# Optimization experiments

Hardware: AMD Instinct MI355X
Metric: run time of the kernel (lower is better)

Reference implementation:

```python
import jax, jax.numpy as jnp
import numpy as np

B, T, C, N = 64, 2048, 1, 128  # batch, max seq len, num_conjugates, num_tags


def setup_inputs() -> dict:
    key = jax.random.key(0)
    k1, k2, k3, k4, k5 = jax.random.split(key, 5)
    emissions = jax.random.normal(k1, (B, T, C, N), dtype=jnp.float32)
    # ragged lengths in [T//2, T], guaranteed >= 1
    token_sizes = jax.random.randint(k2, (B,), T // 2, T + 1, dtype=jnp.int32)
    # learned CRF parameters (torch init is zeros; use small random for a nontrivial baseline)
    transitions = 0.1 * jax.random.normal(k3, (1, C, N, N), dtype=jnp.float32)
    head_transitions = 0.1 * jax.random.normal(k4, (1, C, N), dtype=jnp.float32)
    last_transitions = 0.1 * jax.random.normal(k5, (1, C, N), dtype=jnp.float32)
    return {
        "emissions": emissions,
        "token_sizes": token_sizes,
        "transitions": transitions,
        "head_transitions": head_transitions,
        "last_transitions": last_transitions,
    }


def _log_partition(emissions, transitions, head_transitions, last_transitions, token_sizes):
    # emissions: [B, T, C, N]; transitions: [1, C, N, N]; head/last: [1, C, N]
    trans = transitions[0]  # [C, N, N]
    # alpha_0 = head_transitions (*) emissions[0] in the Log semiring
    alpha0 = head_transitions[0][None, :, :] + emissions[:, 0]  # [B, C, N]

    def step(alpha, inp):
        em_t, t = inp  # em_t: [B, C, N], t: scalar time index
        # Log-semiring matmul: logsumexp over previous tag
        new = jax.nn.logsumexp(alpha[:, :, :, None] + trans[None, :, :, :], axis=2) + em_t
        valid = (t < token_sizes)[:, None, None]  # mask padded steps (identity in semiring)
        return jnp.where(valid, new, alpha), None

    step = jax.checkpoint(step)
    xs = (jnp.swapaxes(emissions[:, 1:], 0, 1), jnp.arange(1, emissions.shape[1]))
    alpha, _ = jax.lax.scan(step, alpha0, xs)
    # terminate with last_transitions, reduce over final tag
    return jax.nn.logsumexp(alpha + last_transitions[0][None, :, :], axis=-1)  # [B, C]


def reference(emissions, token_sizes, transitions, head_transitions, last_transitions):
    return _log_partition(emissions, transitions, head_transitions, last_transitions, token_sizes)
```

## Files before the change

kernel.cpp:

```cpp
#include <hip/hip_runtime.h>
#include <stdint.h>

#define T_LEN 2048
#define B_TOT 64
#define N_TAG 128
#define MID 1024

typedef __attribute__((ext_vector_type(4))) float f32x4;
typedef __attribute__((ext_vector_type(8))) short bf16x8;
typedef __attribute__((ext_vector_type(4))) uint32_t u32x4;
typedef __attribute__((ext_vector_type(2))) uint32_t u32x2;

template <int S>
struct IC {
  static constexpr int value = S;
};

__device__ __align__(16) float g_alpha[B_TOT][N_TAG];
__device__ __align__(16) float g_v[B_TOT][N_TAG];
__device__ float g_Lf[B_TOT];
__device__ float g_Lb[B_TOT];
__device__ int g_done = 0;

__device__ __forceinline__ uint32_t pack2_bf16(float a, float b) {
  uint32_t ua = __float_as_uint(a) + 0x8000u;
  uint32_t ub = __float_as_uint(b) + 0x8000u;
  return __builtin_amdgcn_perm(ua, ub, 0x03020706u);
}

__global__ __launch_bounds__(512, 2) void crf_scan_kernel(
    const float* __restrict__ em, const int* __restrict__ lens,
    const float* __restrict__ trans, const float* __restrict__ head,
    const float* __restrict__ last, float* __restrict__ out) {
  const int lane = threadIdx.x & 63;
  const int w = threadIdx.x >> 6;
  const int f = w >> 1;
  const int h = w & 1;
  const int c = lane & 15;
  const int q = lane >> 4;
  const bool is_fwd = (blockIdx.x < 4);
  const int bg = ((int)blockIdx.x & 3) * 16 + c;
  const int jbase = f * 32 + q * 8 + h * 4;

  __shared__ uint32_t x_lds[2][4][64][4];
  __shared__ int k_lds[16];
  __shared__ int ticket_lds;

  const float* eptr = em + (size_t)bg * T_LEN * N_TAG + jbase;
  f32x4 eslot[8];
  auto issue_eem = [&](auto sc, int row) {
    constexpr int S = decltype(sc)::value;
    eslot[S] = *(const f32x4*)(eptr + (size_t)row * N_TAG);
  };

  const f32x4 vzero = {0.f, 0.f, 0.f, 0.f};

  if (is_fwd) {
    bf16x8 efrag[4];
    {
      const int j = f * 32 + (c >> 2) * 8 + h * 4 + (c & 3);
#pragma unroll
      for (int ktv = 0; ktv < 4; ++ktv) {
        const int ktp = (w + ktv) & 3;
        u32x4 wd;
#pragma unroll
        for (int p = 0; p < 4; ++p) {
          const int i0 = ktp * 32 + q * 8 + 2 * p;
          wd[p] = pack2_bf16(__expf(trans[(i0 + 0) * N_TAG + j]),
                             __expf(trans[(i0 + 1) * N_TAG + j]));
        }
        efrag[ktv] = __builtin_bit_cast(bf16x8, wd);
      }
    }
    float L = 0.f;
    {
      float v0[4];
#pragma unroll
      for (int r = 0; r < 4; ++r) v0[r] = __expf(head[jbase + r] + eptr[r]);
      u32x2 wd;
      wd[0] = pack2_bf16(v0[0], v0[1]);
      wd[1] = pack2_bf16(v0[2], v0[3]);
      *(u32x2*)&x_lds[0][f][lane][h * 2] = wd;
    }
    if (w == 0 && lane < 16) k_lds[lane] = 0;
    __syncthreads();

    issue_eem(IC<1>{}, 1);
    issue_eem(IC<2>{}, 2);
    issue_eem(IC<3>{}, 3);
    issue_eem(IC<4>{}, 4);
    issue_eem(IC<5>{}, 5);
    issue_eem(IC<6>{}, 6);
    issue_eem(IC<7>{}, 7);

    auto step = [&](auto slotc, int t) {
      constexpr int SLOT = decltype(slotc)::value;
      constexpr int RP = (SLOT + 1) & 1;
      constexpr int WP = SLOT & 1;
      issue_eem(IC<(SLOT + 7) & 7>{}, t + 7);
      int e = 0;
      if ((SLOT & 3) == 1) e = k_lds[c];
      u32x4 bfr[4];
#pragma unroll
      for (int ktv = 0; ktv < 4; ++ktv)
        bfr[ktv] = *(const u32x4*)&x_lds[RP][(w + ktv) & 3][lane][0];
      const f32x4 ev = eslot[SLOT];
      float ff[4];
#pragma unroll
      for (int r = 0; r < 4; ++r) ff[r] = __expf(ev[r]);
      if ((SLOT & 3) == 1) {
        const float sc = __uint_as_float((uint32_t)(127 - e) << 23);
#pragma unroll
        for (int r = 0; r < 4; ++r) ff[r] *= sc;
        L += (float)e * 0.6931471805599453f;
      }
      f32x4 a0 = __builtin_amdgcn_mfma_f32_16x16x32_bf16(
          efrag[0], __builtin_bit_cast(bf16x8, bfr[0]), vzero, 0, 0, 0);
      f32x4 a1 = __builtin_amdgcn_mfma_f32_16x16x32_bf16(
          efrag[2], __builtin_bit_cast(bf16x8, bfr[2]), vzero, 0, 0, 0);
      a0 = __builtin_amdgcn_mfma_f32_16x16x32_bf16(
          efrag[1], __builtin_bit_cast(bf16x8, bfr[1]), a0, 0, 0, 0);
      a1 = __builtin_amdgcn_mfma_f32_16x16x32_bf16(
          efrag[3], __builtin_bit_cast(bf16x8, bfr[3]), a1, 0, 0, 0);
      const f32x4 acc = a0 + a1;
      if ((SLOT & 3) == 0) {
        if (w == 0 && lane < 16)
          k_lds[c] = (int)(__float_as_uint(acc[0]) >> 23) - 126;
      }
      if (t == MID - 1) {
#pragma unroll
        for (int r = 0; r < 4; ++r) g_alpha[bg][jbase + r] = acc[r] * ff[r];
        if (w == 0 && q == 0) g_Lf[bg] = L;
      }
      u32x2 wd;
      wd[0] = pack2_bf16(acc[0] * ff[0], acc[1] * ff[1]);
      wd[1] = pack2_bf16(acc[2] * ff[2], acc[3] * ff[3]);
      *(u32x2*)&x_lds[WP][f][lane][h * 2] = wd;
      __syncthreads();
    };

    int t = 1;
#pragma unroll 1
    for (int it = 0; it < 127; ++it) {
      step(IC<1>{}, t);
      step(IC<2>{}, t + 1);
      step(IC<3>{}, t + 2);
      step(IC<4>{}, t + 3);
      step(IC<5>{}, t + 4);
      step(IC<6>{}, t + 5);
      step(IC<7>{}, t + 6);
      step(IC<0>{}, t + 7);
      t += 8;
    }
    step(IC<1>{}, t);
    step(IC<2>{}, t + 1);
    step(IC<3>{}, t + 2);
    step(IC<4>{}, t + 3);
    step(IC<5>{}, t + 4);
    step(IC<6>{}, t + 5);
    step(IC<7>{}, t + 6);
  } else {
    bf16x8 efrag[4];
    {
      const int irow = f * 32 + (c >> 2) * 8 + h * 4 + (c & 3);
#pragma unroll
      for (int ktv = 0; ktv < 4; ++ktv) {
        const int ktp = (w + ktv) & 3;
        u32x4 wd;
#pragma unroll
        for (int p = 0; p < 4; ++p) {
          const int j0 = ktp * 32 + q * 8 + 2 * p;
          wd[p] = pack2_bf16(__expf(trans[irow * N_TAG + j0 + 0]),
                             __expf(trans[irow * N_TAG + j0 + 1]));
        }
        efrag[ktv] = __builtin_bit_cast(bf16x8, wd);
      }
    }
    const int mylen = lens[bg];
    float L = 0.f;
    float vprev[4];
    {
#pragma unroll
      for (int r = 0; r < 4; ++r) vprev[r] = __expf(last[jbase + r]);
      float e0[4];
#pragma unroll
      for (int r = 0; r < 4; ++r)
        e0[r] = __expf(eptr[(size_t)(T_LEN - 1) * N_TAG + r]);
      u32x2 wd;
      wd[0] = pack2_bf16(vprev[0] * e0[0], vprev[1] * e0[1]);
      wd[1] = pack2_bf16(vprev[2] * e0[2], vprev[3] * e0[3]);
      *(u32x2*)&x_lds[0][f][lane][h * 2] = wd;
    }
    if (w == 0 && lane < 16) k_lds[lane] = 0;
    __syncthreads();

    issue_eem(IC<1>{}, T_LEN - 2);
    issue_eem(IC<2>{}, T_LEN - 3);
    issue_eem(IC<3>{}, T_LEN - 4);
    issue_eem(IC<4>{}, T_LEN - 5);
    issue_eem(IC<5>{}, T_LEN - 6);
    issue_eem(IC<6>{}, T_LEN - 7);
    issue_eem(IC<7>{}, T_LEN - 8);

    auto step = [&](auto slotc, int t) {
      constexpr int SLOT = decltype(slotc)::value;
      constexpr int RP = (SLOT + 1) & 1;
      constexpr int WP = SLOT & 1;
      issue_eem(IC<(SLOT + 7) & 7>{}, t - 8);
      int e = 0;
      if ((SLOT & 3) == 1) e = k_lds[c];
      u32x4 bfr[4];
#pragma unroll
      for (int ktv = 0; ktv < 4; ++ktv)
        bfr[ktv] = *(const u32x4*)&x_lds[RP][(w + ktv) & 3][lane][0];
      const f32x4 ev = eslot[SLOT];
      float ee[4];
#pragma unroll
      for (int r = 0; r < 4; ++r) ee[r] = __expf(ev[r]);
      f32x4 a0 = __builtin_amdgcn_mfma_f32_16x16x32_bf16(
          efrag[0], __builtin_bit_cast(bf16x8, bfr[0]), vzero, 0, 0, 0);
      f32x4 a1 = __builtin_amdgcn_mfma_f32_16x16x32_bf16(
          efrag[2], __builtin_bit_cast(bf16x8, bfr[2]), vzero, 0, 0, 0);
      a0 = __builtin_amdgcn_mfma_f32_16x16x32_bf16(
          efrag[1], __builtin_bit_cast(bf16x8, bfr[1]), a0, 0, 0, 0);
      a1 = __builtin_amdgcn_mfma_f32_16x16x32_bf16(
          efrag[3], __builtin_bit_cast(bf16x8, bfr[3]), a1, 0, 0, 0);
      const f32x4 acc = a0 + a1;
      const bool valid = (t < mylen);
      float vnew[4];
#pragma unroll
      for (int r = 0; r < 4; ++r) vnew[r] = valid ? acc[r] : vprev[r];
      if ((SLOT & 3) == 1) {
        const float sc = __uint_as_float((uint32_t)(127 - e) << 23);
#pragma unroll
        for (int r = 0; r < 4; ++r) vnew[r] *= sc;
        L += (float)e * 0.6931471805599453f;
      }
      if ((SLOT & 3) == 0) {
        if (w == 0 && lane < 16)
          k_lds[c] = (int)(__float_as_uint(vnew[0]) >> 23) - 126;
      }
      if (t == MID) {
#pragma unroll
        for (int r = 0; r < 4; ++r) g_v[bg][jbase + r] = vnew[r];
        if (w == 0 && q == 0) g_Lb[bg] = L;
      }
      u32x2 wd;
      wd[0] = pack2_bf16(vnew[0] * ee[0], vnew[1] * ee[1]);
      wd[1] = pack2_bf16(vnew[2] * ee[2], vnew[3] * ee[3]);
      *(u32x2*)&x_lds[WP][f][lane][h * 2] = wd;
#pragma unroll
      for (int r = 0; r < 4; ++r) vprev[r] = vnew[r];
      __syncthreads();
    };

    int t = T_LEN - 1;
#pragma unroll 1
    for (int it = 0; it < 128; ++it) {
      step(IC<1>{}, t);
      step(IC<2>{}, t - 1);
      step(IC<3>{}, t - 2);
      step(IC<4>{}, t - 3);
      step(IC<5>{}, t - 4);
      step(IC<6>{}, t - 5);
      step(IC<7>{}, t - 6);
      step(IC<0>{}, t - 7);
      t -= 8;
    }
  }

  __threadfence();
  if (threadIdx.x == 0) ticket_lds = atomicAdd(&g_done, 1);
  __syncthreads();
  if (ticket_lds == 7) {
    __threadfence();
    const int b = threadIdx.x >> 3;
    const int p = threadIdx.x & 7;
    float s = 0.f;
#pragma unroll
    for (int k = 0; k < 4; ++k) {
      const f32x4 a = *(const f32x4*)&g_alpha[b][p * 16 + k * 4];
      const f32x4 v = *(const f32x4*)&g_v[b][p * 16 + k * 4];
      s += a[0] * v[0] + a[1] * v[1] + a[2] * v[2] + a[3] * v[3];
    }
    s += __shfl_xor(s, 1);
    s += __shfl_xor(s, 2);
    s += __shfl_xor(s, 4);
    if (p == 0) out[b] = __logf(s) + g_Lf[b] + g_Lb[b];
    __syncthreads();
    if (threadIdx.x == 0) atomicExch(&g_done, 0);
  }
}

extern "C" void kernel_launch(void* const* d_in, const int* in_sizes, int n_in,
                              void* d_out, int out_size, void* d_ws,
                              size_t ws_size, hipStream_t stream) {
  const float* em = (const float*)d_in[0];
  const int* lens = (const int*)d_in[1];
  const float* trans = (const float*)d_in[2];
  const float* head = (const float*)d_in[3];
  const float* last = (const float*)d_in[4];
  float* out = (float*)d_out;
  (void)d_ws;
  (void)ws_size;

  crf_scan_kernel<<<8, 512, 0, stream>>>(em, lens, trans, head, last, out);
}
```

Before: 341.6 us.

## Precompute exp(emissions) as bf16 in producer blocks overlapped with the scan

Adds 256 producer blocks to the launch. They exponentiate emissions, pack them to bf16 into a workspace laid out time-major, and publish per-chunk completion counters. The 8 scan blocks spin-wait on those counters and then load the half-size precomputed values, which removes the per-step exp and halves the streamed bytes on the serial critical path. The risks are spin-wait stalls if the producers fall behind, possible deadlock if a scan block waits on producers that are not yet resident, and extra bf16 rounding of the emission factors.

Measured after the change: 395.1 us. 1.16x slower.

```diff
diff --git a/kernel.cpp b/kernel.cpp
--- a/kernel.cpp
+++ b/kernel.cpp
@@ -21,17 +21,52 @@
 __device__ float g_Lf[B_TOT];
 __device__ float g_Lb[B_TOT];
 __device__ int g_done = 0;
+__device__ int g_chunk_rows[16];
 
 __device__ __forceinline__ uint32_t pack2_bf16(float a, float b) {
   uint32_t ua = __float_as_uint(a) + 0x8000u;
   uint32_t ub = __float_as_uint(b) + 0x8000u;
   return __builtin_amdgcn_perm(ua, ub, 0x03020706u);
 }
-
-__global__ __launch_bounds__(512, 2) void crf_scan_kernel(
+__device__ __forceinline__ float bf_lo(uint32_t w) {
+  return __uint_as_float(w << 16);
+}
+__device__ __forceinline__ float bf_hi(uint32_t w) {
+  return __uint_as_float(w & 0xffff0000u);
+}
+
+__global__ __launch_bounds__(512, 2) void crf_fused_kernel(
     const float* __restrict__ em, const int* __restrict__ lens,
     const float* __restrict__ trans, const float* __restrict__ head,
-    const float* __restrict__ last, float* __restrict__ out) {
+    const float* __restrict__ last, uint32_t* __restrict__ eem,
+    float* __restrict__ out) {
+  if (blockIdx.x >= 8) {
+    const int p = (int)blockIdx.x - 8;
+    const int start = (p & 1) ? 2040 - (p >> 1) * 8 : (p >> 1) * 8;
+    const int tid = threadIdx.x;
+#pragma unroll 1
+    for (int u = 0; u < 16; ++u) {
+      const int row = start + (u >> 1);
+      const int unit = (u & 1) * 512 + tid;
+      const int b = unit >> 4;
+      const int kk = unit & 15;
+      const float4* src =
+          (const float4*)(em + ((size_t)b * T_LEN + row) * N_TAG + kk * 8);
+      const float4 p0 = src[0];
+      const float4 p1 = src[1];
+      u32x4 o;
+      o[0] = pack2_bf16(__expf(p0.x), __expf(p0.y));
+      o[1] = pack2_bf16(__expf(p0.z), __expf(p0.w));
+      o[2] = pack2_bf16(__expf(p1.x), __expf(p1.y));
+      o[3] = pack2_bf16(__expf(p1.z), __expf(p1.w));
+      *(u32x4*)(eem + (size_t)row * 4096 + b * 64 + kk * 4) = o;
+    }
+    __syncthreads();
+    __threadfence();
+    if (tid == 0) atomicAdd(&g_chunk_rows[start >> 7], 8);
+    return;
+  }
+
   const int lane = threadIdx.x & 63;
   const int w = threadIdx.x >> 6;
   const int f = w >> 1;
@@ -46,11 +81,21 @@
   __shared__ int k_lds[16];
   __shared__ int ticket_lds;
 
+  auto wait_chunk = [&](int ch) {
+    if (threadIdx.x == 0) {
+      while (__hip_atomic_load(&g_chunk_rows[ch], __ATOMIC_ACQUIRE,
+                               __HIP_MEMORY_SCOPE_AGENT) < 128) {
+      }
+    }
+    __syncthreads();
+  };
+
   const float* eptr = em + (size_t)bg * T_LEN * N_TAG + jbase;
-  f32x4 eslot[8];
+  const uint32_t* eqp = eem + (size_t)bg * 64 + f * 16 + q * 4 + h * 2;
+  u32x2 eslot[8];
   auto issue_eem = [&](auto sc, int row) {
     constexpr int S = decltype(sc)::value;
-    eslot[S] = *(const f32x4*)(eptr + (size_t)row * N_TAG);
+    eslot[S] = *(const u32x2*)(eqp + (size_t)row * 4096);
   };
 
   const f32x4 vzero = {0.f, 0.f, 0.f, 0.f};
@@ -85,6 +130,7 @@
     if (w == 0 && lane < 16) k_lds[lane] = 0;
     __syncthreads();
 
+    wait_chunk(0);
     issue_eem(IC<1>{}, 1);
     issue_eem(IC<2>{}, 2);
     issue_eem(IC<3>{}, 3);
@@ -104,10 +150,12 @@
 #pragma unroll
       for (int ktv = 0; ktv < 4; ++ktv)
         bfr[ktv] = *(const u32x4*)&x_lds[RP][(w + ktv) & 3][lane][0];
-      const f32x4 ev = eslot[SLOT];
+      const u32x2 ev = eslot[SLOT];
       float ff[4];
-#pragma unroll
-      for (int r = 0; r < 4; ++r) ff[r] = __expf(ev[r]);
+      ff[0] = bf_lo(ev[0]);
+      ff[1] = bf_hi(ev[0]);
+      ff[2] = bf_lo(ev[1]);
+      ff[3] = bf_hi(ev[1]);
       if ((SLOT & 3) == 1) {
         const float sc = __uint_as_float((uint32_t)(127 - e) << 23);
 #pragma unroll
@@ -140,8 +188,14 @@
     };
 
     int t = 1;
+    int cur_ch = 0;
 #pragma unroll 1
     for (int it = 0; it < 127; ++it) {
+      const int ch = (15 + 8 * it) >> 7;
+      if (ch != cur_ch) {
+        wait_chunk(ch);
+        cur_ch = ch;
+      }
       step(IC<1>{}, t);
       step(IC<2>{}, t + 1);
       step(IC<3>{}, t + 2);
@@ -152,6 +206,7 @@
       step(IC<0>{}, t + 7);
       t += 8;
     }
+    wait_chunk(8);
     step(IC<1>{}, t);
     step(IC<2>{}, t + 1);
     step(IC<3>{}, t + 2);
@@ -194,6 +249,7 @@
     if (w == 0 && lane < 16) k_lds[lane] = 0;
     __syncthreads();
 
+    wait_chunk(15);
     issue_eem(IC<1>{}, T_LEN - 2);
     issue_eem(IC<2>{}, T_LEN - 3);
     issue_eem(IC<3>{}, T_LEN - 4);
@@ -213,10 +269,12 @@
 #pragma unroll
       for (int ktv = 0; ktv < 4; ++ktv)
         bfr[ktv] = *(const u32x4*)&x_lds[RP][(w + ktv) & 3][lane][0];
-      const f32x4 ev = eslot[SLOT];
+      const u32x2 ev = eslot[SLOT];
       float ee[4];
-#pragma unroll
-      for (int r = 0; r < 4; ++r) ee[r] = __expf(ev[r]);
+      ee[0] = bf_lo(ev[0]);
+      ee[1] = bf_hi(ev[0]);
+      ee[2] = bf_lo(ev[1]);
+      ee[3] = bf_hi(ev[1]);
       f32x4 a0 = __builtin_amdgcn_mfma_f32_16x16x32_bf16(
           efrag[0], __builtin_bit_cast(bf16x8, bfr[0]), vzero, 0, 0, 0);
       f32x4 a1 = __builtin_amdgcn_mfma_f32_16x16x32_bf16(
@@ -255,8 +313,14 @@
     };
 
     int t = T_LEN - 1;
+    int cur_ch = 15;
 #pragma unroll 1
     for (int it = 0; it < 128; ++it) {
+      const int ch = (2032 - 8 * it) >> 7;
+      if (ch != cur_ch) {
+        wait_chunk(ch);
+        cur_ch = ch;
+      }
       step(IC<1>{}, t);
       step(IC<2>{}, t - 1);
       step(IC<3>{}, t - 2);
@@ -288,7 +352,8 @@
     s += __shfl_xor(s, 4);
     if (p == 0) out[b] = __logf(s) + g_Lf[b] + g_Lb[b];
     __syncthreads();
-    if (threadIdx.x == 0) atomicExch(&g_done, 0);
+    if (threadIdx.x == 0) g_done = 0;
+    if (threadIdx.x < 16) g_chunk_rows[threadIdx.x] = 0;
   }
 }
 
@@ -301,8 +366,8 @@
   const float* head = (const float*)d_in[3];
   const float* last = (const float*)d_in[4];
   float* out = (float*)d_out;
-  (void)d_ws;
-  (void)ws_size;
-
-  crf_scan_kernel<<<8, 512, 0, stream>>>(em, lens, trans, head, last, out);
-}
+  uint32_t* ws = (uint32_t*)d_ws;
+
+  crf_fused_kernel<<<264, 512, 0, stream>>>(em, lens, trans, head, last, ws,
+                                            out);
+}
```

## Precompute exp(emissions) as bf16 in a prepass and halve scan block waves

Applied to the files above, without the earlier changes.

Adds a parallel prepass kernel that computes exp of every emission, packs it to bf16 and writes it time-major into the workspace. The sequential scan kernel then loads half the bytes per step and skips the per-step exp. The scan block also drops from 8 to 4 waves, each doing 8 MFMAs per step over 32 tags, so fewer waves take part in each per-step barrier. The costs are an extra launch, a full pass over the emissions, and emission values rounded to bf16 before the multiply.

New measurement: 412.6 us. 1.21x slower.

```diff
diff --git a/kernel.cpp b/kernel.cpp
--- a/kernel.cpp
+++ b/kernel.cpp
@@ -27,41 +27,65 @@
   uint32_t ub = __float_as_uint(b) + 0x8000u;
   return __builtin_amdgcn_perm(ua, ub, 0x03020706u);
 }
-
-__global__ __launch_bounds__(512, 2) void crf_scan_kernel(
+__device__ __forceinline__ float bf_lo(uint32_t w) {
+  return __uint_as_float(w << 16);
+}
+__device__ __forceinline__ float bf_hi(uint32_t w) {
+  return __uint_as_float(w & 0xffff0000u);
+}
+
+__global__ __launch_bounds__(256) void eem_prepass(const float* __restrict__ em,
+                                                   uint32_t* __restrict__ ws) {
+  const int tid = blockIdx.x * blockDim.x + threadIdx.x;
+  const int b = tid >> 15;
+  const int rem = tid & 32767;
+  const int t = rem >> 4;
+  const int kk = rem & 15;
+  const float4* src =
+      (const float4*)(em + ((size_t)b * T_LEN + t) * N_TAG + kk * 8);
+  const float4 p0 = src[0];
+  const float4 p1 = src[1];
+  u32x4 o;
+  o[0] = pack2_bf16(__expf(p0.x), __expf(p0.y));
+  o[1] = pack2_bf16(__expf(p0.z), __expf(p0.w));
+  o[2] = pack2_bf16(__expf(p1.x), __expf(p1.y));
+  o[3] = pack2_bf16(__expf(p1.z), __expf(p1.w));
+  *(u32x4*)(ws + ((size_t)t * B_TOT + b) * (N_TAG / 2) + kk * 4) = o;
+}
+
+__global__ __launch_bounds__(256, 1) void crf_scan_kernel(
     const float* __restrict__ em, const int* __restrict__ lens,
     const float* __restrict__ trans, const float* __restrict__ head,
-    const float* __restrict__ last, float* __restrict__ out) {
+    const float* __restrict__ last, const uint32_t* __restrict__ eem,
+    float* __restrict__ out) {
   const int lane = threadIdx.x & 63;
   const int w = threadIdx.x >> 6;
-  const int f = w >> 1;
-  const int h = w & 1;
   const int c = lane & 15;
   const int q = lane >> 4;
   const bool is_fwd = (blockIdx.x < 4);
   const int bg = ((int)blockIdx.x & 3) * 16 + c;
-  const int jbase = f * 32 + q * 8 + h * 4;
+  const int jb = w * 32 + q * 8;
 
   __shared__ uint32_t x_lds[2][4][64][4];
   __shared__ int k_lds[16];
   __shared__ int ticket_lds;
 
-  const float* eptr = em + (size_t)bg * T_LEN * N_TAG + jbase;
-  f32x4 eslot[8];
+  const uint32_t* eqp = eem + (size_t)bg * 64 + w * 16 + q * 4;
+  u32x4 eslot[8];
   auto issue_eem = [&](auto sc, int row) {
     constexpr int S = decltype(sc)::value;
-    eslot[S] = *(const f32x4*)(eptr + (size_t)row * N_TAG);
+    eslot[S] = *(const u32x4*)(eqp + (size_t)row * 4096);
   };
 
   const f32x4 vzero = {0.f, 0.f, 0.f, 0.f};
 
   if (is_fwd) {
-    bf16x8 efrag[4];
-    {
-      const int j = f * 32 + (c >> 2) * 8 + h * 4 + (c & 3);
-#pragma unroll
-      for (int ktv = 0; ktv < 4; ++ktv) {
-        const int ktp = (w + ktv) & 3;
+    bf16x8 efrag[2][4];
+#pragma unroll
+    for (int mt = 0; mt < 2; ++mt) {
+      const int j = w * 32 + (c >> 2) * 8 + mt * 4 + (c & 3);
+#pragma unroll
+      for (int ktp = 0; ktp < 4; ++ktp) {
         u32x4 wd;
 #pragma unroll
         for (int p = 0; p < 4; ++p) {
@@ -69,18 +93,19 @@
           wd[p] = pack2_bf16(__expf(trans[(i0 + 0) * N_TAG + j]),
                              __expf(trans[(i0 + 1) * N_TAG + j]));
         }
-        efrag[ktv] = __builtin_bit_cast(bf16x8, wd);
+        efrag[mt][ktp] = __builtin_bit_cast(bf16x8, wd);
       }
     }
     float L = 0.f;
     {
-      float v0[4];
-#pragma unroll
-      for (int r = 0; r < 4; ++r) v0[r] = __expf(head[jbase + r] + eptr[r]);
-      u32x2 wd;
-      wd[0] = pack2_bf16(v0[0], v0[1]);
-      wd[1] = pack2_bf16(v0[2], v0[3]);
-      *(u32x2*)&x_lds[0][f][lane][h * 2] = wd;
+      const float* emb = em + (size_t)bg * T_LEN * N_TAG;
+      float v0[8];
+#pragma unroll
+      for (int r = 0; r < 8; ++r) v0[r] = __expf(head[jb + r] + emb[jb + r]);
+      u32x4 wd;
+#pragma unroll
+      for (int d = 0; d < 4; ++d) wd[d] = pack2_bf16(v0[2 * d], v0[2 * d + 1]);
+      *(u32x4*)&x_lds[0][w][lane][0] = wd;
     }
     if (w == 0 && lane < 16) k_lds[lane] = 0;
     __syncthreads();
@@ -97,45 +122,74 @@
       constexpr int SLOT = decltype(slotc)::value;
       constexpr int RP = (SLOT + 1) & 1;
       constexpr int WP = SLOT & 1;
-      issue_eem(IC<(SLOT + 7) & 7>{}, t + 7);
+      {
+        int row = t + 7;
+        if (row > T_LEN - 1) row = T_LEN - 1;
+        issue_eem(IC<(SLOT + 7) & 7>{}, row);
+      }
       int e = 0;
       if ((SLOT & 3) == 1) e = k_lds[c];
       u32x4 bfr[4];
 #pragma unroll
       for (int ktv = 0; ktv < 4; ++ktv)
         bfr[ktv] = *(const u32x4*)&x_lds[RP][(w + ktv) & 3][lane][0];
-      const f32x4 ev = eslot[SLOT];
-      float ff[4];
-#pragma unroll
-      for (int r = 0; r < 4; ++r) ff[r] = __expf(ev[r]);
+      const u32x4 ev = eslot[SLOT];
+      float ff[8];
+#pragma unroll
+      for (int d = 0; d < 4; ++d) {
+        ff[2 * d] = bf_lo(ev[d]);
+        ff[2 * d + 1] = bf_hi(ev[d]);
+      }
       if ((SLOT & 3) == 1) {
         const float sc = __uint_as_float((uint32_t)(127 - e) << 23);
 #pragma unroll
-        for (int r = 0; r < 4; ++r) ff[r] *= sc;
+        for (int r = 0; r < 8; ++r) ff[r] *= sc;
         L += (float)e * 0.6931471805599453f;
       }
-      f32x4 a0 = __builtin_amdgcn_mfma_f32_16x16x32_bf16(
-          efrag[0], __builtin_bit_cast(bf16x8, bfr[0]), vzero, 0, 0, 0);
-      f32x4 a1 = __builtin_amdgcn_mfma_f32_16x16x32_bf16(
-          efrag[2], __builtin_bit_cast(bf16x8, bfr[2]), vzero, 0, 0, 0);
-      a0 = __builtin_amdgcn_mfma_f32_16x16x32_bf16(
-          efrag[1], __builtin_bit_cast(bf16x8, bfr[1]), a0, 0, 0, 0);
-      a1 = __builtin_amdgcn_mfma_f32_16x16x32_bf16(
-          efrag[3], __builtin_bit_cast(bf16x8, bfr[3]), a1, 0, 0, 0);
-      const f32x4 acc = a0 + a1;
+      f32x4 x0 = __builtin_amdgcn_mfma_f32_16x16x32_bf16(
+          efrag[0][(w + 0) & 3], __builtin_bit_cast(bf16x8, bfr[0]), vzero, 0,
+          0, 0);
+      f32x4 y0 = __builtin_amdgcn_mfma_f32_16x16x32_bf16(
+          efrag[0][(w + 2) & 3], __builtin_bit_cast(bf16x8, bfr[2]), vzero, 0,
+          0, 0);
+      f32x4 x1 = __builtin_amdgcn_mfma_f32_16x16x32_bf16(
+          efrag[1][(w + 0) & 3], __builtin_bit_cast(bf16x8, bfr[0]), vzero, 0,
+          0, 0);
+      f32x4 y1 = __builtin_amdgcn_mfma_f32_16x16x32_bf16(
+          efrag[1][(w + 2) & 3], __builtin_bit_cast(bf16x8, bfr[2]), vzero, 0,
+          0, 0);
+      x0 = __builtin_amdgcn_mfma_f32_16x16x32_bf16(
+          efrag[0][(w + 1) & 3], __builtin_bit_cast(bf16x8, bfr[1]), x0, 0, 0,
+          0);
+      y0 = __builtin_amdgcn_mfma_f32_16x16x32_bf16(
+          efrag[0][(w + 3) & 3], __builtin_bit_cast(bf16x8, bfr[3]), y0, 0, 0,
+          0);
+      x1 = __builtin_amdgcn_mfma_f32_16x16x32_bf16(
+          efrag[1][(w + 1) & 3], __builtin_bit_cast(bf16x8, bfr[1]), x1, 0, 0,
+          0);
+      y1 = __builtin_amdgcn_mfma_f32_16x16x32_bf16(
+          efrag[1][(w + 3) & 3], __builtin_bit_cast(bf16x8, bfr[3]), y1, 0, 0,
+          0);
+      const f32x4 a0 = x0 + y0;
+      const f32x4 a1 = x1 + y1;
       if ((SLOT & 3) == 0) {
         if (w == 0 && lane < 16)
-          k_lds[c] = (int)(__float_as_uint(acc[0]) >> 23) - 126;
+          k_lds[c] = (int)(__float_as_uint(a0[0]) >> 23) - 126;
       }
       if (t == MID - 1) {
 #pragma unroll
-        for (int r = 0; r < 4; ++r) g_alpha[bg][jbase + r] = acc[r] * ff[r];
-        if (w == 0 && q == 0) g_Lf[bg] = L;
-      }
-      u32x2 wd;
-      wd[0] = pack2_bf16(acc[0] * ff[0], acc[1] * ff[1]);
-      wd[1] = pack2_bf16(acc[2] * ff[2], acc[3] * ff[3]);
-      *(u32x2*)&x_lds[WP][f][lane][h * 2] = wd;
+        for (int r = 0; r < 4; ++r) {
+          g_alpha[bg][jb + r] = a0[r] * ff[r];
+          g_alpha[bg][jb + 4 + r] = a1[r] * ff[4 + r];
+        }
+        if (w == 0 && lane < 16) g_Lf[bg] = L;
+      }
+      u32x4 wd;
+      wd[0] = pack2_bf16(a0[0] * ff[0], a0[1] * ff[1]);
+      wd[1] = pack2_bf16(a0[2] * ff[2], a0[3] * ff[3]);
+      wd[2] = pack2_bf16(a1[0] * ff[4], a1[1] * ff[5]);
+      wd[3] = pack2_bf16(a1[2] * ff[6], a1[3] * ff[7]);
+      *(u32x4*)&x_lds[WP][w][lane][0] = wd;
       __syncthreads();
     };
 
@@ -160,12 +214,12 @@
     step(IC<6>{}, t + 5);
     step(IC<7>{}, t + 6);
   } else {
-    bf16x8 efrag[4];
-    {
-      const int irow = f * 32 + (c >> 2) * 8 + h * 4 + (c & 3);
-#pragma unroll
-      for (int ktv = 0; ktv < 4; ++ktv) {
-        const int ktp = (w + ktv) & 3;
+    bf16x8 efrag[2][4];
+#pragma unroll
+    for (int mt = 0; mt < 2; ++mt) {
+      const int irow = w * 32 + (c >> 2) * 8 + mt * 4 + (c & 3);
+#pragma unroll
+      for (int ktp = 0; ktp < 4; ++ktp) {
         u32x4 wd;
 #pragma unroll
         for (int p = 0; p < 4; ++p) {
@@ -173,23 +227,22 @@
           wd[p] = pack2_bf16(__expf(trans[irow * N_TAG + j0 + 0]),
                              __expf(trans[irow * N_TAG + j0 + 1]));
         }
-        efrag[ktv] = __builtin_bit_cast(bf16x8, wd);
+        efrag[mt][ktp] = __builtin_bit_cast(bf16x8, wd);
       }
     }
     const int mylen = lens[bg];
     float L = 0.f;
-    float vprev[4];
+    float vprev[8];
     {
 #pragma unroll
-      for (int r = 0; r < 4; ++r) vprev[r] = __expf(last[jbase + r]);
-      float e0[4];
-#pragma unroll
-      for (int r = 0; r < 4; ++r)
-        e0[r] = __expf(eptr[(size_t)(T_LEN - 1) * N_TAG + r]);
-      u32x2 wd;
-      wd[0] = pack2_bf16(vprev[0] * e0[0], vprev[1] * e0[1]);
-      wd[1] = pack2_bf16(vprev[2] * e0[2], vprev[3] * e0[3]);
-      *(u32x2*)&x_lds[0][f][lane][h * 2] = wd;
+      for (int r = 0; r < 8; ++r) vprev[r] = __expf(last[jb + r]);
+      const u32x4 e0 = *(const u32x4*)(eqp + (size_t)(T_LEN - 1) * 4096);
+      u32x4 wd;
+#pragma unroll
+      for (int d = 0; d < 4; ++d)
+        wd[d] = pack2_bf16(vprev[2 * d] * bf_lo(e0[d]),
+                           vprev[2 * d + 1] * bf_hi(e0[d]));
+      *(u32x4*)&x_lds[0][w][lane][0] = wd;
     }
     if (w == 0 && lane < 16) k_lds[lane] = 0;
     __syncthreads();
@@ -213,27 +266,50 @@
 #pragma unroll
       for (int ktv = 0; ktv < 4; ++ktv)
         bfr[ktv] = *(const u32x4*)&x_lds[RP][(w + ktv) & 3][lane][0];
-      const f32x4 ev = eslot[SLOT];
-      float ee[4];
-#pragma unroll
-      for (int r = 0; r < 4; ++r) ee[r] = __expf(ev[r]);
-      f32x4 a0 = __builtin_amdgcn_mfma_f32_16x16x32_bf16(
-          efrag[0], __builtin_bit_cast(bf16x8, bfr[0]), vzero, 0, 0, 0);
-      f32x4 a1 = __builtin_amdgcn_mfma_f32_16x16x32_bf16(
-          efrag[2], __builtin_bit_cast(bf16x8, bfr[2]), vzero, 0, 0, 0);
-      a0 = __builtin_amdgcn_mfma_f32_16x16x32_bf16(
-          efrag[1], __builtin_bit_cast(bf16x8, bfr[1]), a0, 0, 0, 0);
-      a1 = __builtin_amdgcn_mfma_f32_16x16x32_bf16(
-          efrag[3], __builtin_bit_cast(bf16x8, bfr[3]), a1, 0, 0, 0);
-      const f32x4 acc = a0 + a1;
+      const u32x4 ev = eslot[SLOT];
+      float ee[8];
+#pragma unroll
+      for (int d = 0; d < 4; ++d) {
+        ee[2 * d] = bf_lo(ev[d]);
+        ee[2 * d + 1] = bf_hi(ev[d]);
+      }
+      f32x4 x0 = __builtin_amdgcn_mfma_f32_16x16x32_bf16(
+          efrag[0][(w + 0) & 3], __builtin_bit_cast(bf16x8, bfr[0]), vzero, 0,
+          0, 0);
+      f32x4 y0 = __builtin_amdgcn_mfma_f32_16x16x32_bf16(
+          efrag[0][(w + 2) & 3], __builtin_bit_cast(bf16x8, bfr[2]), vzero, 0,
+          0, 0);
+      f32x4 x1 = __builtin_amdgcn_mfma_f32_16x16x32_bf16(
+          efrag[1][(w + 0) & 3], __builtin_bit_cast(bf16x8, bfr[0]), vzero, 0,
+          0, 0);
+      f32x4 y1 = __builtin_amdgcn_mfma_f32_16x16x32_bf16(
+          efrag[1][(w + 2) & 3], __builtin_bit_cast(bf16x8, bfr[2]), vzero, 0,
+          0, 0);
+      x0 = __builtin_amdgcn_mfma_f32_16x16x32_bf16(
+          efrag[0][(w + 1) & 3], __builtin_bit_cast(bf16x8, bfr[1]), x0, 0, 0,
+          0);
+      y0 = __builtin_amdgcn_mfma_f32_16x16x32_bf16(
+          efrag[0][(w + 3) & 3], __builtin_bit_cast(bf16x8, bfr[3]), y0, 0, 0,
+          0);
+      x1 = __builtin_amdgcn_mfma_f32_16x16x32_bf16(
+          efrag[1][(w + 1) & 3], __builtin_bit_cast(bf16x8, bfr[1]), x1, 0, 0,
+          0);
+      y1 = __builtin_amdgcn_mfma_f32_16x16x32_bf16(
+          efrag[1][(w + 3) & 3], __builtin_bit_cast(bf16x8, bfr[3]), y1, 0, 0,
+          0);
+      const f32x4 a0 = x0 + y0;
+      const f32x4 a1 = x1 + y1;
       const bool valid = (t < mylen);
-      float vnew[4];
-#pragma unroll
-      for (int r = 0; r < 4; ++r) vnew[r] = valid ? acc[r] : vprev[r];
+      float vnew[8];
+#pragma unroll
+      for (int r = 0; r < 4; ++r) {
+        vnew[r] = valid ? a0[r] : vprev[r];
+        vnew[4 + r] = valid ? a1[r] : vprev[4 + r];
+      }
       if ((SLOT & 3) == 1) {
         const float sc = __uint_as_float((uint32_t)(127 - e) << 23);
 #pragma unroll
-        for (int r = 0; r < 4; ++r) vnew[r] *= sc;
+        for (int r = 0; r < 8; ++r) vnew[r] *= sc;
         L += (float)e * 0.6931471805599453f;
       }
       if ((SLOT & 3) == 0) {
@@ -242,15 +318,17 @@
       }
       if (t == MID) {
 #pragma unroll
-        for (int r = 0; r < 4; ++r) g_v[bg][jbase + r] = vnew[r];
-        if (w == 0 && q == 0) g_Lb[bg] = L;
-      }
-      u32x2 wd;
-      wd[0] = pack2_bf16(vnew[0] * ee[0], vnew[1] * ee[1]);
-      wd[1] = pack2_bf16(vnew[2] * ee[2], vnew[3] * ee[3]);
-      *(u32x2*)&x_lds[WP][f][lane][h * 2] = wd;
-#pragma unroll
-      for (int r = 0; r < 4; ++r) vprev[r] = vnew[r];
+        for (int r = 0; r < 8; ++r) g_v[bg][jb + r] = vnew[r];
+        if (w == 0 && lane < 16) g_Lb[bg] = L;
+      }
+      u32x4 wd;
+#pragma unroll
+      for (int d = 0; d < 4; ++d)
+        wd[d] = pack2_bf16(vnew[2 * d] * ee[2 * d],
+                           vnew[2 * d + 1] * ee[2 * d + 1]);
+      *(u32x4*)&x_lds[WP][w][lane][0] = wd;
+#pragma unroll
+      for (int r = 0; r < 8; ++r) vprev[r] = vnew[r];
       __syncthreads();
     };
 
@@ -274,21 +352,20 @@
   __syncthreads();
   if (ticket_lds == 7) {
     __threadfence();
-    const int b = threadIdx.x >> 3;
-    const int p = threadIdx.x & 7;
+    const int b = threadIdx.x >> 2;
+    const int p = threadIdx.x & 3;
     float s = 0.f;
 #pragma unroll
-    for (int k = 0; k < 4; ++k) {
-      const f32x4 a = *(const f32x4*)&g_alpha[b][p * 16 + k * 4];
-      const f32x4 v = *(const f32x4*)&g_v[b][p * 16 + k * 4];
+    for (int k = 0; k < 8; ++k) {
+      const f32x4 a = *(const f32x4*)&g_alpha[b][p * 32 + k * 4];
+      const f32x4 v = *(const f32x4*)&g_v[b][p * 32 + k * 4];
       s += a[0] * v[0] + a[1] * v[1] + a[2] * v[2] + a[3] * v[3];
     }
     s += __shfl_xor(s, 1);
     s += __shfl_xor(s, 2);
-    s += __shfl_xor(s, 4);
     if (p == 0) out[b] = __logf(s) + g_Lf[b] + g_Lb[b];
     __syncthreads();
-    if (threadIdx.x == 0) atomicExch(&g_done, 0);
+    if (threadIdx.x == 0) g_done = 0;
   }
 }
 
@@ -301,8 +378,8 @@
   const float* head = (const float*)d_in[3];
   const float* last = (const float*)d_in[4];
   float* out = (float*)d_out;
-  (void)d_ws;
-  (void)ws_size;
-
-  crf_scan_kernel<<<8, 512, 0, stream>>>(em, lens, trans, head, last, out);
-}
+  uint32_t* ws = (uint32_t*)d_ws;
+
+  eem_prepass<<<8192, 256, 0, stream>>>(em, ws);
+  crf_scan_kernel<<<8, 256, 0, stream>>>(em, lens, trans, head, last, ws, out);
+}
```
